# Optimization experiments

Measured on AMD Instinct MI355X. Metric: run time of the kernel, lower is better.

Reference implementation:

```python
import jax, jax.numpy as jnp
import numpy as np

B, S, D, H = 4, 2048, 1024, 16
HD = D // H  # head dim = 64

def setup_inputs() -> dict:
    key = jax.random.key(0)
    k1, k2, k3 = jax.random.split(key, 3)
    x = jax.random.normal(k1, (B, S, D), dtype=jnp.float32)
    W_attn = jax.random.normal(k2, (D, 3 * D), dtype=jnp.float32) * 0.02
    b_attn = jnp.zeros((3 * D,), dtype=jnp.float32)
    W_proj = jax.random.normal(k3, (D, D), dtype=jnp.float32) * 0.02
    b_proj = jnp.zeros((D,), dtype=jnp.float32)
    return {"x": x, "W_attn": W_attn, "b_attn": b_attn, "W_proj": W_proj, "b_proj": b_proj}

def reference(x, W_attn, b_attn, W_proj, b_proj):
    b, s, d = x.shape
    qkv = x @ W_attn + b_attn                       # [b, s, 3d]
    q, k, v = jnp.split(qkv, 3, axis=-1)
    # [b, s, d] -> [b, h, s, hd]
    def heads(t):
        return t.reshape(b, s, H, HD).transpose(0, 2, 1, 3)
    q, k, v = heads(q), heads(k), heads(v)
    scale = 1.0 / jnp.sqrt(jnp.asarray(HD, dtype=x.dtype))
    scores = jnp.einsum('bhqd,bhkd->bhqk', q, k) * scale  # [b, h, s, s]
    causal = jnp.tril(jnp.ones((s, s), dtype=bool))
    scores = jnp.where(causal[None, None, :, :], scores, jnp.asarray(-jnp.inf, dtype=x.dtype))
    attn = jax.nn.softmax(scores, axis=-1)
    out = jnp.einsum('bhqk,bhkd->bhqd', attn, v)    # [b, h, s, hd]
    out = out.transpose(0, 2, 1, 3).reshape(b, s, d)
    return out @ W_proj + b_proj
```

## Files before the change

kernel.cpp:

```cpp
#include <hip/hip_runtime.h>
#include <hip/hip_bf16.h>
#include <stdint.h>

#define B_  4
#define S_  2048
#define D_  1024
#define H_  16
#define HD_ 64

typedef __attribute__((ext_vector_type(8))) short          s16x8;
typedef __attribute__((ext_vector_type(4))) float          f32x4;
typedef __attribute__((ext_vector_type(8))) unsigned short u16x8;

__device__ __forceinline__ unsigned short f2bf(float f) {
  union { float f; unsigned int u; } v; v.f = f;
  unsigned int u = v.u;
  u += 0x7fffu + ((u >> 16) & 1u);
  return (unsigned short)(u >> 16);
}

#define GLDS16(g, l)                                                           \
  __builtin_amdgcn_global_load_lds(                                            \
      (const __attribute__((address_space(1))) void*)(g),                      \
      (__attribute__((address_space(3))) void*)(l), 16, 0, 0)

__global__ void k_cvt(const float* __restrict__ src, unsigned short* __restrict__ dst, int n4) {
  int i = blockIdx.x * blockDim.x + threadIdx.x;
  int stride = gridDim.x * blockDim.x;
  for (int j = i; j < n4; j += stride) {
    float4 v = reinterpret_cast<const float4*>(src)[j];
    ushort4 o;
    o.x = f2bf(v.x); o.y = f2bf(v.y); o.z = f2bf(v.z); o.w = f2bf(v.w);
    reinterpret_cast<ushort4*>(dst)[j] = o;
  }
}

__global__ void k_tpose_cvt(const float* __restrict__ src, unsigned short* __restrict__ dst,
                            int R, int C) {
  __shared__ unsigned short tile[64][72];
  int c0 = blockIdx.x * 64, r0 = blockIdx.y * 64;
  int tx = threadIdx.x & 63, ty = threadIdx.x >> 6;
#pragma unroll
  for (int i = 0; i < 16; ++i) {
    int r = ty * 16 + i;
    tile[r][tx] = f2bf(src[(size_t)(r0 + r) * C + c0 + tx]);
  }
  __syncthreads();
#pragma unroll
  for (int i = 0; i < 16; ++i) {
    int c = ty * 16 + i;
    dst[(size_t)(c0 + c) * R + r0 + tx] = tile[tx][c];
  }
}

__global__ void k_tpose_v(const unsigned short* __restrict__ src, unsigned short* __restrict__ dst) {
  __shared__ unsigned short tile[64][72];
  int s0 = blockIdx.x * 64, bh = blockIdx.y;
  int tx = threadIdx.x & 63, ty = threadIdx.x >> 6;
  const unsigned short* sb = src + (size_t)bh * S_ * HD_;
  unsigned short*       db = dst + (size_t)bh * S_ * HD_;
#pragma unroll
  for (int i = 0; i < 16; ++i) {
    int r = ty * 16 + i;
    tile[r][tx] = sb[(size_t)(s0 + r) * HD_ + tx];
  }
  __syncthreads();
#pragma unroll
  for (int i = 0; i < 16; ++i) {
    int hd = ty * 16 + i;
    db[(size_t)hd * S_ + s0 + tx] = tile[tx][hd];
  }
}

__device__ __forceinline__ void gemm_core(const unsigned short* __restrict__ A,
                                          const unsigned short* __restrict__ Bt,
                                          int K, int m0, int n0,
                                          unsigned short* sm, f32x4 acc[4][4]) {
  const int t = threadIdx.x;
  const int w = t >> 6, l = t & 63;
  const int wm = w >> 1, wn = w & 1;
  const int lo = l & 15, hi = l >> 4;

  const int ci0 = w * 64 + l, ci1 = ci0 + 256;
  const int rA0 = ci0 >> 2, cA0 = (ci0 & 3) ^ ((rA0 >> 1) & 3);
  const int rA1 = ci1 >> 2, cA1 = (ci1 & 3) ^ ((rA1 >> 1) & 3);
  const unsigned short* gA0 = A  + (size_t)(m0 + rA0) * K + cA0 * 8;
  const unsigned short* gA1 = A  + (size_t)(m0 + rA1) * K + cA1 * 8;
  const unsigned short* gB0 = Bt + (size_t)(n0 + rA0) * K + cA0 * 8;
  const unsigned short* gB1 = Bt + (size_t)(n0 + rA1) * K + cA1 * 8;
  const int ldsA0 = (w * 64) * 8;
  const int ldsA1 = (256 + w * 64) * 8;

#pragma unroll
  for (int m = 0; m < 4; ++m)
#pragma unroll
    for (int n = 0; n < 4; ++n)
      acc[m][n] = (f32x4){0.f, 0.f, 0.f, 0.f};

  const int NT = K >> 5;

  {
    unsigned short* b = sm;
    GLDS16(gA0, b + ldsA0);
    GLDS16(gA1, b + ldsA1);
    GLDS16(gB0, b + 4096 + ldsA0);
    GLDS16(gB1, b + 4096 + ldsA1);
  }

  for (int kt = 0; kt < NT; ++kt) {
    __syncthreads();
    if (kt + 1 < NT) {
      unsigned short* b = sm + ((kt + 1) & 1) * 8192;
      const int ko = (kt + 1) << 5;
      GLDS16(gA0 + ko, b + ldsA0);
      GLDS16(gA1 + ko, b + ldsA1);
      GLDS16(gB0 + ko, b + 4096 + ldsA0);
      GLDS16(gB1 + ko, b + 4096 + ldsA1);
    }
    const unsigned short* Ab = sm + (kt & 1) * 8192;
    const unsigned short* Bb = Ab + 4096;
    s16x8 af[4], bfr[4];
#pragma unroll
    for (int m = 0; m < 4; ++m) {
      int row = wm * 64 + m * 16 + lo;
      af[m] = *(const s16x8*)(Ab + row * 32 + ((hi ^ ((row >> 1) & 3)) << 3));
    }
#pragma unroll
    for (int n = 0; n < 4; ++n) {
      int row = wn * 64 + n * 16 + lo;
      bfr[n] = *(const s16x8*)(Bb + row * 32 + ((hi ^ ((row >> 1) & 3)) << 3));
    }
    __builtin_amdgcn_s_setprio(1);
#pragma unroll
    for (int m = 0; m < 4; ++m)
#pragma unroll
      for (int n = 0; n < 4; ++n)
        acc[m][n] = __builtin_amdgcn_mfma_f32_16x16x32_bf16(af[m], bfr[n], acc[m][n], 0, 0, 0);
    __builtin_amdgcn_s_setprio(0);
  }
}

__global__ __launch_bounds__(256, 3)
void k_gemm_qkv(const unsigned short* __restrict__ A, const unsigned short* __restrict__ Bt,
                const float* __restrict__ bias,
                unsigned short* __restrict__ Qh, unsigned short* __restrict__ Kh,
                unsigned short* __restrict__ Vh) {
  __shared__ unsigned short sm[2 * 8192];
  const int m0 = blockIdx.y * 128, n0 = blockIdx.x * 128;
  f32x4 acc[4][4];
  gemm_core(A, Bt, 1024, m0, n0, sm, acc);
  const int t = threadIdx.x, w = t >> 6, l = t & 63;
  const int wm = w >> 1, wn = w & 1, lo = l & 15, hi = l >> 4;
#pragma unroll
  for (int m = 0; m < 4; ++m)
#pragma unroll
    for (int n = 0; n < 4; ++n) {
      int col = n0 + wn * 64 + n * 16 + lo;
      float bv = bias[col];
      int sel = col >> 10, cw = col & 1023, h = cw >> 6, hd = cw & 63;
      float scl = (sel == 0) ? 0.18033688011112042f : 1.0f;
      unsigned short* dst = (sel == 0) ? Qh : ((sel == 1) ? Kh : Vh);
#pragma unroll
      for (int r = 0; r < 4; ++r) {
        int row = m0 + wm * 64 + m * 16 + hi * 4 + r;
        int b = row >> 11, s = row & 2047;
        dst[(((size_t)b * H_ + h) * S_ + s) * HD_ + hd] = f2bf((acc[m][n][r] + bv) * scl);
      }
    }
}

__global__ __launch_bounds__(256, 3)
void k_gemm_proj(const unsigned short* __restrict__ A, const unsigned short* __restrict__ Bt,
                 const float* __restrict__ bias, float* __restrict__ C, int N) {
  __shared__ unsigned short sm[2 * 8192];
  const int m0 = blockIdx.y * 128, n0 = blockIdx.x * 128;
  f32x4 acc[4][4];
  gemm_core(A, Bt, 1024, m0, n0, sm, acc);
  const int t = threadIdx.x, w = t >> 6, l = t & 63;
  const int wm = w >> 1, wn = w & 1, lo = l & 15, hi = l >> 4;
#pragma unroll
  for (int m = 0; m < 4; ++m)
#pragma unroll
    for (int n = 0; n < 4; ++n) {
      int col = n0 + wn * 64 + n * 16 + lo;
      float bv = bias[col];
#pragma unroll
      for (int r = 0; r < 4; ++r) {
        int row = m0 + wm * 64 + m * 16 + hi * 4 + r;
        C[(size_t)row * N + col] = acc[m][n][r] + bv;
      }
    }
}

__global__ __launch_bounds__(256, 2)
void k_attn(const unsigned short* __restrict__ Qh, const unsigned short* __restrict__ Kh,
            const unsigned short* __restrict__ Vt, unsigned short* __restrict__ ctx) {
  __shared__ unsigned short Kl[2 * 4096];
  __shared__ unsigned short Vl[2 * 4096];
  const int bid = blockIdx.x;
  const int g8  = bid & 7;
  const int idx = bid >> 3;
  const int bh  = g8 * 8 + (idx & 7);
  const int jp  = idx >> 3;
  const int t = threadIdx.x, w = t >> 6, l = t & 63, lo = l & 15, hi = l >> 4;
  const unsigned short* Qb = Qh + (size_t)bh * S_ * HD_;
  const unsigned short* Kb = Kh + (size_t)bh * S_ * HD_;
  const unsigned short* Vb = Vt + (size_t)bh * S_ * HD_;
  const int bb = bh >> 4, h = bh & 15;

  const int r0s = t >> 3, schunk = t & 7, r1s = r0s + 32;
  const int ks0 = ((r0s & 1) << 4) | ((r0s >> 1) & 15);
  const int ks1 = 32 | ((r1s & 1) << 4) | ((r1s >> 1) & 15);
  const int kd0 = ks0 * 64 + 8 * (schunk ^ (ks0 & 7));
  const int kd1 = ks1 * 64 + 8 * (schunk ^ (ks1 & 7));
  const int vd0 = r0s * 64 + 8 * (schunk ^ (r0s & 7));
  const int vd1 = r1s * 64 + 8 * (schunk ^ (r1s & 7));
  const unsigned short* ksrc0 = Kb + r0s * HD_ + schunk * 8;
  const unsigned short* ksrc1 = Kb + r1s * HD_ + schunk * 8;
  const unsigned short* vsrc0 = Vb + (size_t)r0s * S_ + schunk * 8;
  const unsigned short* vsrc1 = Vb + (size_t)r1s * S_ + schunk * 8;

  const int e0 = jp + 1;
  const int nt = 32 - jp;

  s16x8 qf[2][2];
  int qbase[2];
  qbase[0] = 64 * jp        + w * 16;
  qbase[1] = 64 * (31 - jp) + w * 16;
#pragma unroll
  for (int g = 0; g < 2; ++g)
#pragma unroll
    for (int kk = 0; kk < 2; ++kk)
      qf[g][kk] = *(const s16x8*)(Qb + (size_t)(qbase[g] + lo) * HD_ + kk * 32 + hi * 8);

  f32x4 O[2][4];
#pragma unroll
  for (int g = 0; g < 2; ++g)
#pragma unroll
    for (int nh = 0; nh < 4; ++nh) O[g][nh] = (f32x4){0.f, 0.f, 0.f, 0.f};
  float mrun[2] = {-1e30f, -1e30f}, lrun[2] = {0.f, 0.f};

  u16x8 rk0 = *(const u16x8*)ksrc0, rk1 = *(const u16x8*)ksrc1;
  u16x8 rv0 = *(const u16x8*)vsrc0, rv1 = *(const u16x8*)vsrc1;
  *(u16x8*)&Kl[kd0] = rk0;
  *(u16x8*)&Kl[kd1] = rk1;
  *(u16x8*)&Vl[vd0] = rv0;
  *(u16x8*)&Vl[vd1] = rv1;
  __syncthreads();

  for (int kt = 0; kt < nt; ++kt) {
    const int kv0 = kt * 64;
    const int cb = (kt & 1) * 4096;
    const bool pf = (kt + 1 < nt);
    const bool g0act = (kt < e0);
    if (pf) {
      rk0 = *(const u16x8*)(ksrc0 + (size_t)(kv0 + 64) * HD_);
      rk1 = *(const u16x8*)(ksrc1 + (size_t)(kv0 + 64) * HD_);
      rv0 = *(const u16x8*)(vsrc0 + kv0 + 64);
      rv1 = *(const u16x8*)(vsrc1 + kv0 + 64);
    }

    f32x4 p[2][4];
#pragma unroll
    for (int g = 0; g < 2; ++g)
#pragma unroll
      for (int n = 0; n < 4; ++n) p[g][n] = (f32x4){0.f, 0.f, 0.f, 0.f};
#pragma unroll
    for (int kk = 0; kk < 2; ++kk) {
      s16x8 kf[4];
#pragma unroll
      for (int n = 0; n < 4; ++n)
        kf[n] = *(const s16x8*)&Kl[cb + (n * 16 + lo) * 64 + 8 * ((kk * 4 + hi) ^ (lo & 7))];
      __builtin_amdgcn_s_setprio(1);
#pragma unroll
      for (int n = 0; n < 4; ++n)
        p[1][n] = __builtin_amdgcn_mfma_f32_16x16x32_bf16(kf[n], qf[1][kk], p[1][n], 0, 0, 0);
      if (g0act) {
#pragma unroll
        for (int n = 0; n < 4; ++n)
          p[0][n] = __builtin_amdgcn_mfma_f32_16x16x32_bf16(kf[n], qf[0][kk], p[0][n], 0, 0, 0);
      }
      __builtin_amdgcn_s_setprio(0);
    }

    union PU { unsigned int u[4]; s16x8 s; };
    PU pa[2][2];
#pragma unroll
    for (int g = 0; g < 2; ++g) {
      if (g == 0 && !g0act) continue;
      if (kv0 + 63 > qbase[g]) {
        const int q = qbase[g] + lo;
#pragma unroll
        for (int n = 0; n < 4; ++n)
#pragma unroll
          for (int r = 0; r < 4; ++r) {
            int kv = kv0 + 32 * (n >> 1) + 8 * hi + 2 * r + (n & 1);
            p[g][n][r] = (kv <= q) ? p[g][n][r] : -1e30f;
          }
      }
      float mx = fmaxf(fmaxf(fmaxf(p[g][0][0], p[g][0][1]), fmaxf(p[g][0][2], p[g][0][3])),
                       fmaxf(fmaxf(p[g][1][0], p[g][1][1]), fmaxf(p[g][1][2], p[g][1][3])));
      mx = fmaxf(mx, fmaxf(fmaxf(fmaxf(p[g][2][0], p[g][2][1]), fmaxf(p[g][2][2], p[g][2][3])),
                           fmaxf(fmaxf(p[g][3][0], p[g][3][1]), fmaxf(p[g][3][2], p[g][3][3]))));
      mx = fmaxf(mx, __shfl_xor(mx, 16));
      mx = fmaxf(mx, __shfl_xor(mx, 32));
      const bool need = !__all(mx <= mrun[g] + 8.0f);
      if (need) {
        float mnew = fmaxf(mrun[g], mx);
        float alpha = exp2f(mrun[g] - mnew);
        mrun[g] = mnew;
        lrun[g] *= alpha;
#pragma unroll
        for (int r = 0; r < 4; ++r) {
          float ar_ = __shfl(alpha, 4 * hi + r);
#pragma unroll
          for (int nh = 0; nh < 4; ++nh) O[g][nh][r] *= ar_;
        }
      }
      float sum = 0.f;
#pragma unroll
      for (int n = 0; n < 4; ++n)
#pragma unroll
        for (int r = 0; r < 4; ++r) {
          float e = exp2f(p[g][n][r] - mrun[g]);
          p[g][n][r] = e;
          sum += e;
        }
      sum += __shfl_xor(sum, 16);
      sum += __shfl_xor(sum, 32);
      lrun[g] += sum;
#pragma unroll
      for (int c = 0; c < 2; ++c)
#pragma unroll
        for (int r = 0; r < 4; ++r) {
          unsigned int pk;
          asm("v_cvt_pk_bf16_f32 %0, %1, %2"
              : "=v"(pk) : "v"(p[g][2 * c][r]), "v"(p[g][2 * c + 1][r]));
          pa[g][c].u[r] = pk;
        }
    }

#pragma unroll
    for (int c = 0; c < 2; ++c) {
      s16x8 vf[4];
#pragma unroll
      for (int nh = 0; nh < 4; ++nh)
        vf[nh] = *(const s16x8*)&Vl[cb + (nh * 16 + lo) * 64 + 8 * ((4 * c + hi) ^ (lo & 7))];
      __builtin_amdgcn_s_setprio(1);
#pragma unroll
      for (int nh = 0; nh < 4; ++nh)
        O[1][nh] = __builtin_amdgcn_mfma_f32_16x16x32_bf16(pa[1][c].s, vf[nh], O[1][nh], 0, 0, 0);
      if (g0act) {
#pragma unroll
        for (int nh = 0; nh < 4; ++nh)
          O[0][nh] = __builtin_amdgcn_mfma_f32_16x16x32_bf16(pa[0][c].s, vf[nh], O[0][nh], 0, 0, 0);
      }
      __builtin_amdgcn_s_setprio(0);
    }

    if (pf) {
      const int db = ((kt + 1) & 1) * 4096;
      *(u16x8*)&Kl[db + kd0] = rk0;
      *(u16x8*)&Kl[db + kd1] = rk1;
      *(u16x8*)&Vl[db + vd0] = rv0;
      *(u16x8*)&Vl[db + vd1] = rv1;
      __syncthreads();
    }
  }

#pragma unroll
  for (int g = 0; g < 2; ++g) {
#pragma unroll
    for (int r = 0; r < 4; ++r) {
      float li = 1.0f / __shfl(lrun[g], 4 * hi + r);
      int qg = qbase[g] + 4 * hi + r;
#pragma unroll
      for (int nh = 0; nh < 4; ++nh) {
        int hd = nh * 16 + lo;
        ctx[(((size_t)(bb * S_ + qg)) * H_ + h) * HD_ + hd] = f2bf(O[g][nh][r] * li);
      }
    }
  }
}

extern "C" void kernel_launch(void* const* d_in, const int* in_sizes, int n_in,
                              void* d_out, int out_size, void* d_ws, size_t ws_size,
                              hipStream_t stream) {
  const float* x      = (const float*)d_in[0];
  const float* W_attn = (const float*)d_in[1];
  const float* b_attn = (const float*)d_in[2];
  const float* W_proj = (const float*)d_in[3];
  const float* b_proj = (const float*)d_in[4];
  float* out = (float*)d_out;

  char* ws = (char*)d_ws;
  size_t off = 0;
  auto alloc = [&](size_t bytes) {
    char* p = ws + off;
    off += (bytes + 255) & ~(size_t)255;
    return p;
  };
  unsigned short* xb  = (unsigned short*)alloc((size_t)8192 * 1024 * 2);
  unsigned short* Wta = (unsigned short*)alloc((size_t)3072 * 1024 * 2);
  unsigned short* Wtp = (unsigned short*)alloc((size_t)1024 * 1024 * 2);
  unsigned short* Qh  = (unsigned short*)alloc((size_t)64 * 2048 * 64 * 2);
  unsigned short* Kh  = (unsigned short*)alloc((size_t)64 * 2048 * 64 * 2);
  unsigned short* Vh  = (unsigned short*)alloc((size_t)64 * 2048 * 64 * 2);
  unsigned short* Vt  = (unsigned short*)alloc((size_t)64 * 2048 * 64 * 2);
  unsigned short* ctx = (unsigned short*)alloc((size_t)8192 * 1024 * 2);

  k_cvt<<<dim3(2048), dim3(256), 0, stream>>>(x, xb, (8192 * 1024) / 4);
  k_tpose_cvt<<<dim3(48, 16), dim3(256), 0, stream>>>(W_attn, Wta, 1024, 3072);
  k_tpose_cvt<<<dim3(16, 16), dim3(256), 0, stream>>>(W_proj, Wtp, 1024, 1024);
  k_gemm_qkv<<<dim3(24, 64), dim3(256), 0, stream>>>(xb, Wta, b_attn, Qh, Kh, Vh);
  k_tpose_v<<<dim3(32, 64), dim3(256), 0, stream>>>(Vh, Vt);
  k_attn<<<dim3(1024), dim3(256), 0, stream>>>(Qh, Kh, Vt, ctx);
  k_gemm_proj<<<dim3(8, 64), dim3(256), 0, stream>>>(ctx, Wtp, b_proj, out, 1024);
}
```

Measured before the change: 199.3 us.

## Process two KV tiles per barrier step with single-buffered 128-row staging

Restructures the attention loop so each iteration stages two 64-row K/V tiles into both LDS buffers and processes them back-to-back, with prefetch of the next 128 rows held in registers. This halves the number of loop iterations and the exposed global-load issue points per tile. In exchange it drops the double-buffering: a full barrier is now needed before overwriting LDS plus one after, giving two syncs per 128 rows instead of one per 64, and register pressure grows from the eight prefetch vectors.

```diff
diff --git a/kernel.cpp b/kernel.cpp
--- a/kernel.cpp
+++ b/kernel.cpp
@@ -220,8 +220,9 @@
   const unsigned short* vsrc0 = Vb + (size_t)r0s * S_ + schunk * 8;
   const unsigned short* vsrc1 = Vb + (size_t)r1s * S_ + schunk * 8;
 
-  const int e0 = jp + 1;
-  const int nt = 32 - jp;
+  const int e0  = jp + 1;
+  const int ex1 = 32 - jp;
+  const int nv  = (ex1 + 1) >> 1;
 
   s16x8 qf[2][2];
   int qbase[2];
@@ -240,26 +241,9 @@
     for (int nh = 0; nh < 4; ++nh) O[g][nh] = (f32x4){0.f, 0.f, 0.f, 0.f};
   float mrun[2] = {-1e30f, -1e30f}, lrun[2] = {0.f, 0.f};
 
-  u16x8 rk0 = *(const u16x8*)ksrc0, rk1 = *(const u16x8*)ksrc1;
-  u16x8 rv0 = *(const u16x8*)vsrc0, rv1 = *(const u16x8*)vsrc1;
-  *(u16x8*)&Kl[kd0] = rk0;
-  *(u16x8*)&Kl[kd1] = rk1;
-  *(u16x8*)&Vl[vd0] = rv0;
-  *(u16x8*)&Vl[vd1] = rv1;
-  __syncthreads();
-
-  for (int kt = 0; kt < nt; ++kt) {
-    const int kv0 = kt * 64;
-    const int cb = (kt & 1) * 4096;
-    const bool pf = (kt + 1 < nt);
-    const bool g0act = (kt < e0);
-    if (pf) {
-      rk0 = *(const u16x8*)(ksrc0 + (size_t)(kv0 + 64) * HD_);
-      rk1 = *(const u16x8*)(ksrc1 + (size_t)(kv0 + 64) * HD_);
-      rv0 = *(const u16x8*)(vsrc0 + kv0 + 64);
-      rv1 = *(const u16x8*)(vsrc1 + kv0 + 64);
-    }
-
+  auto process = [&](int kv0, int sub, bool g0act) {
+    const unsigned short* Kbuf = Kl + sub * 4096;
+    const unsigned short* Vbuf = Vl + sub * 4096;
     f32x4 p[2][4];
 #pragma unroll
     for (int g = 0; g < 2; ++g)
@@ -270,7 +254,7 @@
       s16x8 kf[4];
 #pragma unroll
       for (int n = 0; n < 4; ++n)
-        kf[n] = *(const s16x8*)&Kl[cb + (n * 16 + lo) * 64 + 8 * ((kk * 4 + hi) ^ (lo & 7))];
+        kf[n] = *(const s16x8*)&Kbuf[(n * 16 + lo) * 64 + 8 * ((kk * 4 + hi) ^ (lo & 7))];
       __builtin_amdgcn_s_setprio(1);
 #pragma unroll
       for (int n = 0; n < 4; ++n)
@@ -345,7 +329,7 @@
       s16x8 vf[4];
 #pragma unroll
       for (int nh = 0; nh < 4; ++nh)
-        vf[nh] = *(const s16x8*)&Vl[cb + (nh * 16 + lo) * 64 + 8 * ((4 * c + hi) ^ (lo & 7))];
+        vf[nh] = *(const s16x8*)&Vbuf[(nh * 16 + lo) * 64 + 8 * ((4 * c + hi) ^ (lo & 7))];
       __builtin_amdgcn_s_setprio(1);
 #pragma unroll
       for (int nh = 0; nh < 4; ++nh)
@@ -357,13 +341,47 @@
       }
       __builtin_amdgcn_s_setprio(0);
     }
-
+  };
+
+  u16x8 rk00 = *(const u16x8*)ksrc0;
+  u16x8 rk01 = *(const u16x8*)ksrc1;
+  u16x8 rk10 = *(const u16x8*)(ksrc0 + (size_t)64 * HD_);
+  u16x8 rk11 = *(const u16x8*)(ksrc1 + (size_t)64 * HD_);
+  u16x8 rv00 = *(const u16x8*)vsrc0;
+  u16x8 rv01 = *(const u16x8*)vsrc1;
+  u16x8 rv10 = *(const u16x8*)(vsrc0 + 64);
+  u16x8 rv11 = *(const u16x8*)(vsrc1 + 64);
+  *(u16x8*)&Kl[kd0] = rk00;        *(u16x8*)&Kl[kd1] = rk01;
+  *(u16x8*)&Kl[4096 + kd0] = rk10; *(u16x8*)&Kl[4096 + kd1] = rk11;
+  *(u16x8*)&Vl[vd0] = rv00;        *(u16x8*)&Vl[vd1] = rv01;
+  *(u16x8*)&Vl[4096 + vd0] = rv10; *(u16x8*)&Vl[4096 + vd1] = rv11;
+  __syncthreads();
+
+  for (int kt = 0; kt < nv; ++kt) {
+    const int base = kt * 128;
+    const bool pf = (kt + 1 < nv);
     if (pf) {
-      const int db = ((kt + 1) & 1) * 4096;
-      *(u16x8*)&Kl[db + kd0] = rk0;
-      *(u16x8*)&Kl[db + kd1] = rk1;
-      *(u16x8*)&Vl[db + vd0] = rv0;
-      *(u16x8*)&Vl[db + vd1] = rv1;
+      const int nb = base + 128;
+      rk00 = *(const u16x8*)(ksrc0 + (size_t)nb * HD_);
+      rk01 = *(const u16x8*)(ksrc1 + (size_t)nb * HD_);
+      rk10 = *(const u16x8*)(ksrc0 + (size_t)(nb + 64) * HD_);
+      rk11 = *(const u16x8*)(ksrc1 + (size_t)(nb + 64) * HD_);
+      rv00 = *(const u16x8*)(vsrc0 + nb);
+      rv01 = *(const u16x8*)(vsrc1 + nb);
+      rv10 = *(const u16x8*)(vsrc0 + nb + 64);
+      rv11 = *(const u16x8*)(vsrc1 + nb + 64);
+    }
+
+    process(base, 0, 2 * kt < e0);
+    if (2 * kt + 1 < ex1)
+      process(base + 64, 1, 2 * kt + 1 < e0);
+
+    if (pf) {
+      __syncthreads();
+      *(u16x8*)&Kl[kd0] = rk00;        *(u16x8*)&Kl[kd1] = rk01;
+      *(u16x8*)&Kl[4096 + kd0] = rk10; *(u16x8*)&Kl[4096 + kd1] = rk11;
+      *(u16x8*)&Vl[vd0] = rv00;        *(u16x8*)&Vl[vd1] = rv01;
+      *(u16x8*)&Vl[4096 + vd0] = rv10; *(u16x8*)&Vl[4096 + vd1] = rv11;
       __syncthreads();
     }
   }
```

New measurement: 194.4 us. 2.5% less time.
